# Optimization experiments

Hardware: AMD Instinct MI355X
Metric: run time of the kernel (lower is better)

The kernel has to match this reference:

```python
import jax, jax.numpy as jnp
import numpy as np

K = 16  # top-k patches kept (module default)

def setup_inputs() -> dict:
    key = jax.random.key(0)
    ks = jax.random.split(key, 5)
    N, D, A, H = 100000, 1024, 128, 256
    x = jax.random.normal(ks[0], (N, D), dtype=jnp.float32)
    Wa1 = jax.random.normal(ks[1], (D, A), dtype=jnp.float32) * (1.0 / np.sqrt(D))
    ba1 = jnp.zeros((A,), dtype=jnp.float32)
    Wa2 = jax.random.normal(ks[2], (A, 1), dtype=jnp.float32) * (1.0 / np.sqrt(A))
    ba2 = jnp.zeros((1,), dtype=jnp.float32)
    Wc1 = jax.random.normal(ks[3], (D, H), dtype=jnp.float32) * (1.0 / np.sqrt(D))
    bc1 = jnp.zeros((H,), dtype=jnp.float32)
    Wc2 = jax.random.normal(ks[4], (H, 1), dtype=jnp.float32) * (1.0 / np.sqrt(H))
    bc2 = jnp.zeros((1,), dtype=jnp.float32)
    return {"x": x, "Wa1": Wa1, "ba1": ba1, "Wa2": Wa2, "ba2": ba2,
            "Wc1": Wc1, "bc1": bc1, "Wc2": Wc2, "bc2": bc2}

def reference(x, Wa1, ba1, Wa2, ba2, Wc1, bc1, Wc2, bc2):
    # attention logits: Linear -> tanh -> Linear, shape [N]
    scores = (jnp.tanh(x @ Wa1 + ba1) @ Wa2 + ba2)[:, 0]
    # top-k selection over patch dim (k < N here)
    top_vals, top_idx = jax.lax.top_k(scores, K)       # [K], [K]
    x_k = x[top_idx]                                    # [K, D] gather
    attn_w = jax.nn.softmax(top_vals)                   # renormalise over k
    slide_embedding = attn_w @ x_k                      # [D] weighted sum
    # classifier MLP (dropout is identity in eval)
    h = jax.nn.relu(slide_embedding @ Wc1 + bc1)
    logit = (h @ Wc2 + bc2)[0]
    # scatter attention weights back into full-length vector
    full_weights = jnp.zeros(x.shape[0], dtype=x.dtype).at[top_idx].set(attn_w)
    return logit, slide_embedding, full_weights, top_idx
```

## Files before the change

### kernel.cpp

```cpp
#include <hip/hip_runtime.h>
#include <cstddef>
#include <cstdint>

#define N_PATCH 100000
#define D_IN    1024
#define A_DIM   128
#define H_DIM   256
#define KTOP    16

#define OUT_LOGIT 0
#define OUT_EMB   1
#define OUT_FW    (1 + D_IN)
#define OUT_TOPI  (OUT_FW + N_PATCH)

#define WS_SCORES 0
#define WS_CANDV  (N_PATCH)
#define WS_CANDI  (N_PATCH + 4096)
#define WS_ATTN   (N_PATCH + 2 * 4096)
#define WS_TOPI   (WS_ATTN + KTOP)
#define WS_EMB    (WS_TOPI + KTOP)
#define WS_HPART  (WS_EMB + D_IN)
#define WS_WPK    (WS_HPART + 16 * H_DIM)

#define NB2A  256
#define CHUNK 391

typedef __attribute__((ext_vector_type(8))) short bf8_t;
typedef __attribute__((ext_vector_type(4))) float f4_t;

__global__ __launch_bounds__(256) void k_prepack(
    const float* __restrict__ Wa1, uint4* __restrict__ wpk)
{
    int t = blockIdx.x * 256 + threadIdx.x;
    int lane = t & 63;
    int part = (t >> 6) & 1;
    int nt   = (t >> 7) & 7;
    int ks   = t >> 10;
    int n  = nt * 16 + (lane & 15);
    int k0 = ks * 32 + ((lane >> 4) * 8);
    union { ushort u[8]; uint4 v; } o;
    #pragma unroll
    for (int j = 0; j < 8; ++j) {
        float w = Wa1[(size_t)(k0 + j) * A_DIM + n];
        uint b = __float_as_uint(w);
        if (part == 0) {
            o.u[j] = (ushort)(b >> 16);
        } else {
            float hf = __uint_as_float(b & 0xffff0000u);
            o.u[j] = (ushort)(__float_as_uint(w - hf) >> 16);
        }
    }
    wpk[t] = o.v;
}

__device__ __forceinline__ void split8(const float4& a, const float4& b,
                                       bf8_t& hi, bf8_t& lo)
{
    union { float f[8]; uint u[8]; float4 v4[2]; } X;
    X.v4[0] = a; X.v4[1] = b;
    union { uint u[4]; bf8_t v; } H, L;
    #pragma unroll
    for (int j = 0; j < 4; ++j) {
        uint x0 = X.u[2 * j], x1 = X.u[2 * j + 1];
        H.u[j] = __builtin_amdgcn_perm(x1, x0, 0x07060302);
        float l0 = X.f[2 * j]     - __uint_as_float(x0 & 0xffff0000u);
        float l1 = X.f[2 * j + 1] - __uint_as_float(x1 & 0xffff0000u);
        L.u[j] = __builtin_amdgcn_perm(__float_as_uint(l1), __float_as_uint(l0), 0x07060302);
    }
    hi = H.v; lo = L.v;
}

#define MFMA_BF16 __builtin_amdgcn_mfma_f32_16x16x32_bf16

__global__ __launch_bounds__(256) void k_scores(
    const float* __restrict__ x, const uint4* __restrict__ wpk,
    const float* __restrict__ ba1, const float* __restrict__ Wa2,
    const float* __restrict__ ba2, float* __restrict__ scores)
{
    __shared__ uint4 sB[2][1024];

    const int tid = threadIdx.x;
    const int ln  = tid & 63;
    const int q   = ln >> 4;
    const int c   = ln & 15;
    const int wv  = tid >> 6;
    const int row0 = blockIdx.x * 128 + wv * 32;

    const int r0 = min(row0 + c,      N_PATCH - 1);
    const int r1 = min(row0 + 16 + c, N_PATCH - 1);
    const float* pa0 = x + (size_t)r0 * D_IN + q * 8;
    const float* pa1 = x + (size_t)r1 * D_IN + q * 8;

    f4_t acc[2][8];
    #pragma unroll
    for (int rt = 0; rt < 2; ++rt)
        #pragma unroll
        for (int nt = 0; nt < 8; ++nt)
            acc[rt][nt] = (f4_t){0.f, 0.f, 0.f, 0.f};

    uint4 b0[4], bpre[4];
    #pragma unroll
    for (int i = 0; i < 4; ++i) b0[i] = wpk[tid + i * 256];
    #pragma unroll
    for (int i = 0; i < 4; ++i) sB[0][tid + i * 256] = b0[i];
    #pragma unroll
    for (int i = 0; i < 4; ++i) bpre[i] = wpk[1024 + tid + i * 256];

    float4 a_cur[4], a_nxt[4];
    a_cur[0] = *(const float4*)(pa0);
    a_cur[1] = *(const float4*)(pa0 + 4);
    a_cur[2] = *(const float4*)(pa1);
    a_cur[3] = *(const float4*)(pa1 + 4);

    __syncthreads();

    for (int ks = 0; ks < 32; ++ks) {
        const int cur = ks & 1;

        if (ks < 31) {
            #pragma unroll
            for (int i = 0; i < 4; ++i) sB[cur ^ 1][tid + i * 256] = bpre[i];
            a_nxt[0] = *(const float4*)(pa0 + (ks + 1) * 32);
            a_nxt[1] = *(const float4*)(pa0 + (ks + 1) * 32 + 4);
            a_nxt[2] = *(const float4*)(pa1 + (ks + 1) * 32);
            a_nxt[3] = *(const float4*)(pa1 + (ks + 1) * 32 + 4);
        }
        if (ks < 30) {
            #pragma unroll
            for (int i = 0; i < 4; ++i) bpre[i] = wpk[(ks + 2) * 1024 + tid + i * 256];
        }

        bf8_t ahi0, alo0, ahi1, alo1;
        split8(a_cur[0], a_cur[1], ahi0, alo0);
        split8(a_cur[2], a_cur[3], ahi1, alo1);

        const bf8_t* sBf = (const bf8_t*)sB[cur];
        #pragma unroll
        for (int nt = 0; nt < 8; nt += 2) {
            bf8_t bh0 = sBf[(nt * 2 + 0) * 64 + ln];
            bf8_t bl0 = sBf[(nt * 2 + 1) * 64 + ln];
            bf8_t bh1 = sBf[(nt * 2 + 2) * 64 + ln];
            bf8_t bl1 = sBf[(nt * 2 + 3) * 64 + ln];
            acc[0][nt]     = MFMA_BF16(ahi0, bh0, acc[0][nt],     0, 0, 0);
            acc[1][nt]     = MFMA_BF16(ahi1, bh0, acc[1][nt],     0, 0, 0);
            acc[0][nt + 1] = MFMA_BF16(ahi0, bh1, acc[0][nt + 1], 0, 0, 0);
            acc[1][nt + 1] = MFMA_BF16(ahi1, bh1, acc[1][nt + 1], 0, 0, 0);
            acc[0][nt]     = MFMA_BF16(alo0, bh0, acc[0][nt],     0, 0, 0);
            acc[1][nt]     = MFMA_BF16(alo1, bh0, acc[1][nt],     0, 0, 0);
            acc[0][nt + 1] = MFMA_BF16(alo0, bh1, acc[0][nt + 1], 0, 0, 0);
            acc[1][nt + 1] = MFMA_BF16(alo1, bh1, acc[1][nt + 1], 0, 0, 0);
            acc[0][nt]     = MFMA_BF16(ahi0, bl0, acc[0][nt],     0, 0, 0);
            acc[1][nt]     = MFMA_BF16(ahi1, bl0, acc[1][nt],     0, 0, 0);
            acc[0][nt + 1] = MFMA_BF16(ahi0, bl1, acc[0][nt + 1], 0, 0, 0);
            acc[1][nt + 1] = MFMA_BF16(ahi1, bl1, acc[1][nt + 1], 0, 0, 0);
        }

        #pragma unroll
        for (int i = 0; i < 4; ++i) a_cur[i] = a_nxt[i];
        __syncthreads();
    }

    float b1v[8], w2v[8];
    #pragma unroll
    for (int nt = 0; nt < 8; ++nt) {
        b1v[nt] = ba1[nt * 16 + c];
        w2v[nt] = Wa2[nt * 16 + c];
    }
    const float b2 = ba2[0];

    #pragma unroll
    for (int rt = 0; rt < 2; ++rt)
        #pragma unroll
        for (int reg = 0; reg < 4; ++reg) {
            float p = 0.f;
            #pragma unroll
            for (int nt = 0; nt < 8; ++nt)
                p += tanhf(acc[rt][nt][reg] + b1v[nt]) * w2v[nt];
            #pragma unroll
            for (int off = 1; off < 16; off <<= 1)
                p += __shfl_xor(p, off, 64);
            if (c == 0) {
                int row = row0 + rt * 16 + q * 4 + reg;
                if (row < N_PATCH) scores[row] = p + b2;
            }
        }
}

__global__ __launch_bounds__(256) void k_topk_local(
    const float* __restrict__ scores, float* __restrict__ candv,
    int* __restrict__ candi, float* __restrict__ out_fw)
{
    __shared__ float sv[512];
    __shared__ float rv[256];
    __shared__ int   rs[256];
    const int tid  = threadIdx.x;
    const int base = blockIdx.x * CHUNK;

    for (int i = tid; i < 512; i += 256) {
        int g = base + i;
        sv[i] = (i < CHUNK && g < N_PATCH) ? scores[g] : -1e30f;
    }
    for (int i = tid; i < CHUNK; i += 256) {
        int g = base + i;
        if (g < N_PATCH) out_fw[g] = 0.f;
    }
    __syncthreads();

    for (int r = 0; r < KTOP; ++r) {
        float v1 = sv[tid], v2 = sv[tid + 256];
        float bv; int bs;
        if (v2 > v1) { bv = v2; bs = tid + 256; } else { bv = v1; bs = tid; }
        rv[tid] = bv; rs[tid] = bs;
        __syncthreads();
        for (int off = 128; off > 0; off >>= 1) {
            if (tid < off) {
                float ov = rv[tid + off]; int os = rs[tid + off];
                if (ov > rv[tid] || (ov == rv[tid] && os < rs[tid])) {
                    rv[tid] = ov; rs[tid] = os;
                }
            }
            __syncthreads();
        }
        if (tid == 0) {
            int s = rs[0];
            candv[blockIdx.x * KTOP + r] = rv[0];
            candi[blockIdx.x * KTOP + r] = base + s;
            sv[s] = -1e30f;
        }
        __syncthreads();
    }
}

__global__ __launch_bounds__(256) void k_topk_global(
    const float* __restrict__ candv, const int* __restrict__ candi,
    float* __restrict__ out, float* __restrict__ ws_attn, int* __restrict__ ws_topi)
{
    __shared__ float cv[4096];
    __shared__ int   ci[4096];
    __shared__ float rv[256];
    __shared__ int   rgx[256];
    __shared__ int   rsl[256];
    __shared__ float topv[KTOP];
    __shared__ int   topi[KTOP];
    __shared__ float attn[KTOP];
    const int tid = threadIdx.x;

    for (int i = tid; i < 4096; i += 256) { cv[i] = candv[i]; ci[i] = candi[i]; }
    __syncthreads();

    for (int r = 0; r < KTOP; ++r) {
        float bv = -1e38f; int bg = 0x7fffffff; int bs = tid * 16;
        #pragma unroll
        for (int i = 0; i < 16; ++i) {
            int s = tid * 16 + i;
            float v = cv[s]; int g = ci[s];
            if (v > bv || (v == bv && g < bg)) { bv = v; bg = g; bs = s; }
        }
        rv[tid] = bv; rgx[tid] = bg; rsl[tid] = bs;
        __syncthreads();
        for (int off = 128; off > 0; off >>= 1) {
            if (tid < off) {
                if (rv[tid + off] > rv[tid] ||
                    (rv[tid + off] == rv[tid] && rgx[tid + off] < rgx[tid])) {
                    rv[tid] = rv[tid + off]; rgx[tid] = rgx[tid + off]; rsl[tid] = rsl[tid + off];
                }
            }
            __syncthreads();
        }
        if (tid == 0) {
            topv[r] = rv[0]; topi[r] = rgx[0]; cv[rsl[0]] = -1e30f;
        }
        __syncthreads();
    }

    if (tid == 0) {
        float mx = topv[0];
        float s = 0.f;
        for (int k2 = 0; k2 < KTOP; ++k2) {
            float e = expf(topv[k2] - mx);
            attn[k2] = e; s += e;
        }
        float inv = 1.f / s;
        for (int k2 = 0; k2 < KTOP; ++k2) attn[k2] *= inv;
    }
    __syncthreads();

    if (tid < KTOP) {
        out[OUT_TOPI + tid] = (float)topi[tid];
        out[OUT_FW + topi[tid]] = attn[tid];
        ws_attn[tid] = attn[tid];
        ws_topi[tid] = topi[tid];
    }
}

__global__ __launch_bounds__(256) void k_embed(
    const float* __restrict__ x, const float* __restrict__ attn,
    const int* __restrict__ topi, float* __restrict__ out, float* __restrict__ emb)
{
    __shared__ float a[KTOP];
    __shared__ int   ti[KTOP];
    if (threadIdx.x < KTOP) { a[threadIdx.x] = attn[threadIdx.x]; ti[threadIdx.x] = topi[threadIdx.x]; }
    __syncthreads();
    int d = blockIdx.x * 256 + threadIdx.x;
    float e = 0.f;
    #pragma unroll
    for (int k2 = 0; k2 < KTOP; ++k2)
        e = fmaf(a[k2], x[(size_t)ti[k2] * D_IN + d], e);
    out[OUT_EMB + d] = e;
    emb[d] = e;
}

__global__ __launch_bounds__(256) void k_mlp1(
    const float* __restrict__ emb, const float* __restrict__ Wc1,
    float* __restrict__ hpart)
{
    __shared__ float se[64];
    const int b = blockIdx.x, tid = threadIdx.x;
    if (tid < 64) se[tid] = emb[b * 64 + tid];
    __syncthreads();
    float p = 0.f;
    #pragma unroll 8
    for (int d = 0; d < 64; ++d)
        p = fmaf(se[d], Wc1[(size_t)(b * 64 + d) * H_DIM + tid], p);
    hpart[b * H_DIM + tid] = p;
}

__global__ __launch_bounds__(256) void k_logit(
    const float* __restrict__ hpart, const float* __restrict__ bc1,
    const float* __restrict__ Wc2, const float* __restrict__ bc2,
    float* __restrict__ out)
{
    __shared__ float red[256];
    const int tid = threadIdx.x;
    float h = bc1[tid];
    #pragma unroll
    for (int i = 0; i < 16; ++i) h += hpart[i * H_DIM + tid];
    h = fmaxf(h, 0.f) * Wc2[tid];
    red[tid] = h;
    __syncthreads();
    for (int off = 128; off > 0; off >>= 1) {
        if (tid < off) red[tid] += red[tid + off];
        __syncthreads();
    }
    if (tid == 0) out[OUT_LOGIT] = red[0] + bc2[0];
}

extern "C" void kernel_launch(void* const* d_in, const int* in_sizes, int n_in,
                              void* d_out, int out_size, void* d_ws, size_t ws_size,
                              hipStream_t stream)
{
    const float* x   = (const float*)d_in[0];
    const float* Wa1 = (const float*)d_in[1];
    const float* ba1 = (const float*)d_in[2];
    const float* Wa2 = (const float*)d_in[3];
    const float* ba2 = (const float*)d_in[4];
    const float* Wc1 = (const float*)d_in[5];
    const float* bc1 = (const float*)d_in[6];
    const float* Wc2 = (const float*)d_in[7];
    const float* bc2 = (const float*)d_in[8];
    float* out = (float*)d_out;
    float* ws  = (float*)d_ws;

    float* scores = ws + WS_SCORES;
    float* candv  = ws + WS_CANDV;
    int*   candi  = (int*)(ws + WS_CANDI);
    float* attn   = ws + WS_ATTN;
    int*   topi   = (int*)(ws + WS_TOPI);
    float* emb    = ws + WS_EMB;
    float* hpart  = ws + WS_HPART;
    uint4* wpk    = (uint4*)(ws + WS_WPK);

    dim3 blk(256);
    k_prepack<<<128, blk, 0, stream>>>(Wa1, wpk);
    k_scores<<<(N_PATCH + 127) / 128, blk, 0, stream>>>(x, wpk, ba1, Wa2, ba2, scores);
    k_topk_local<<<NB2A, blk, 0, stream>>>(scores, candv, candi, out + OUT_FW);
    k_topk_global<<<1, blk, 0, stream>>>(candv, candi, out, attn, topi);
    k_embed<<<4, blk, 0, stream>>>(x, attn, topi, out, emb);
    k_mlp1<<<16, blk, 0, stream>>>(emb, Wc1, hpart);
    k_logit<<<1, blk, 0, stream>>>(hpart, bc1, Wc2, bc2, out);
}
```

Measured before the change: 776.8 us.

## Unroll score GEMM by two with register double-buffered A loads; fuse tail kernels

Measured after the change: 785.3 us. Within noise of the previous version (+1.1%).

```diff
diff --git a/kernel.cpp b/kernel.cpp
--- a/kernel.cpp
+++ b/kernel.cpp
@@ -16,11 +16,7 @@
 #define WS_SCORES 0
 #define WS_CANDV  (N_PATCH)
 #define WS_CANDI  (N_PATCH + 4096)
-#define WS_ATTN   (N_PATCH + 2 * 4096)
-#define WS_TOPI   (WS_ATTN + KTOP)
-#define WS_EMB    (WS_TOPI + KTOP)
-#define WS_HPART  (WS_EMB + D_IN)
-#define WS_WPK    (WS_HPART + 16 * H_DIM)
+#define WS_WPK    (N_PATCH + 2 * 4096 + 64)
 
 #define NB2A  256
 #define CHUNK 391
@@ -72,6 +68,52 @@
 
 #define MFMA_BF16 __builtin_amdgcn_mfma_f32_16x16x32_bf16
 
+#define BAR_LDS() do {                                          \
+    asm volatile("s_waitcnt lgkmcnt(0)" ::: "memory");          \
+    __builtin_amdgcn_s_barrier();                               \
+    asm volatile("" ::: "memory");                              \
+} while (0)
+
+#define SCORE_STEP(KS, CUR) do {                                               \
+    bf8_t ahi0, alo0, ahi1, alo1;                                              \
+    split8(A##CUR[0], A##CUR[1], ahi0, alo0);                                  \
+    split8(A##CUR[2], A##CUR[3], ahi1, alo1);                                  \
+    if ((KS) < 31) {                                                           \
+        _Pragma("unroll")                                                      \
+        for (int i = 0; i < 4; ++i) sB[(CUR) ^ 1][tid + i * 256] = bpre[i];    \
+    }                                                                          \
+    {                                                                          \
+        const int kp = ((KS) + 2 < 32) ? (KS) + 2 : 31;                        \
+        _Pragma("unroll")                                                      \
+        for (int i = 0; i < 4; ++i) bpre[i] = wpk[kp * 1024 + tid + i * 256];  \
+        A##CUR[0] = *(const float4*)(pa0 + kp * 32);                           \
+        A##CUR[1] = *(const float4*)(pa0 + kp * 32 + 4);                       \
+        A##CUR[2] = *(const float4*)(pa1 + kp * 32);                           \
+        A##CUR[3] = *(const float4*)(pa1 + kp * 32 + 4);                       \
+    }                                                                          \
+    const bf8_t* sBf = (const bf8_t*)sB[CUR];                                  \
+    _Pragma("unroll")                                                          \
+    for (int nt = 0; nt < 8; nt += 2) {                                        \
+        bf8_t bh0 = sBf[(nt * 2 + 0) * 64 + ln];                               \
+        bf8_t bl0 = sBf[(nt * 2 + 1) * 64 + ln];                               \
+        bf8_t bh1 = sBf[(nt * 2 + 2) * 64 + ln];                               \
+        bf8_t bl1 = sBf[(nt * 2 + 3) * 64 + ln];                               \
+        acc[0][nt]     = MFMA_BF16(ahi0, bh0, acc[0][nt],     0, 0, 0);        \
+        acc[1][nt]     = MFMA_BF16(ahi1, bh0, acc[1][nt],     0, 0, 0);        \
+        acc[0][nt + 1] = MFMA_BF16(ahi0, bh1, acc[0][nt + 1], 0, 0, 0);        \
+        acc[1][nt + 1] = MFMA_BF16(ahi1, bh1, acc[1][nt + 1], 0, 0, 0);        \
+        acc[0][nt]     = MFMA_BF16(alo0, bh0, acc[0][nt],     0, 0, 0);        \
+        acc[1][nt]     = MFMA_BF16(alo1, bh0, acc[1][nt],     0, 0, 0);        \
+        acc[0][nt + 1] = MFMA_BF16(alo0, bh1, acc[0][nt + 1], 0, 0, 0);        \
+        acc[1][nt + 1] = MFMA_BF16(alo1, bh1, acc[1][nt + 1], 0, 0, 0);        \
+        acc[0][nt]     = MFMA_BF16(ahi0, bl0, acc[0][nt],     0, 0, 0);        \
+        acc[1][nt]     = MFMA_BF16(ahi1, bl0, acc[1][nt],     0, 0, 0);        \
+        acc[0][nt + 1] = MFMA_BF16(ahi0, bl1, acc[0][nt + 1], 0, 0, 0);        \
+        acc[1][nt + 1] = MFMA_BF16(ahi1, bl1, acc[1][nt + 1], 0, 0, 0);        \
+    }                                                                          \
+    BAR_LDS();                                                                 \
+} while (0)
+
 __global__ __launch_bounds__(256) void k_scores(
     const float* __restrict__ x, const uint4* __restrict__ wpk,
     const float* __restrict__ ba1, const float* __restrict__ Wa2,
@@ -98,66 +140,32 @@
         for (int nt = 0; nt < 8; ++nt)
             acc[rt][nt] = (f4_t){0.f, 0.f, 0.f, 0.f};
 
-    uint4 b0[4], bpre[4];
-    #pragma unroll
-    for (int i = 0; i < 4; ++i) b0[i] = wpk[tid + i * 256];
-    #pragma unroll
-    for (int i = 0; i < 4; ++i) sB[0][tid + i * 256] = b0[i];
+    uint4 bpre[4];
+    {
+        uint4 b0[4];
+        #pragma unroll
+        for (int i = 0; i < 4; ++i) b0[i] = wpk[tid + i * 256];
+        #pragma unroll
+        for (int i = 0; i < 4; ++i) sB[0][tid + i * 256] = b0[i];
+    }
     #pragma unroll
     for (int i = 0; i < 4; ++i) bpre[i] = wpk[1024 + tid + i * 256];
 
-    float4 a_cur[4], a_nxt[4];
-    a_cur[0] = *(const float4*)(pa0);
-    a_cur[1] = *(const float4*)(pa0 + 4);
-    a_cur[2] = *(const float4*)(pa1);
-    a_cur[3] = *(const float4*)(pa1 + 4);
-
-    __syncthreads();
-
-    for (int ks = 0; ks < 32; ++ks) {
-        const int cur = ks & 1;
-
-        if (ks < 31) {
-            #pragma unroll
-            for (int i = 0; i < 4; ++i) sB[cur ^ 1][tid + i * 256] = bpre[i];
-            a_nxt[0] = *(const float4*)(pa0 + (ks + 1) * 32);
-            a_nxt[1] = *(const float4*)(pa0 + (ks + 1) * 32 + 4);
-            a_nxt[2] = *(const float4*)(pa1 + (ks + 1) * 32);
-            a_nxt[3] = *(const float4*)(pa1 + (ks + 1) * 32 + 4);
-        }
-        if (ks < 30) {
-            #pragma unroll
-            for (int i = 0; i < 4; ++i) bpre[i] = wpk[(ks + 2) * 1024 + tid + i * 256];
-        }
-
-        bf8_t ahi0, alo0, ahi1, alo1;
-        split8(a_cur[0], a_cur[1], ahi0, alo0);
-        split8(a_cur[2], a_cur[3], ahi1, alo1);
-
-        const bf8_t* sBf = (const bf8_t*)sB[cur];
-        #pragma unroll
-        for (int nt = 0; nt < 8; nt += 2) {
-            bf8_t bh0 = sBf[(nt * 2 + 0) * 64 + ln];
-            bf8_t bl0 = sBf[(nt * 2 + 1) * 64 + ln];
-            bf8_t bh1 = sBf[(nt * 2 + 2) * 64 + ln];
-            bf8_t bl1 = sBf[(nt * 2 + 3) * 64 + ln];
-            acc[0][nt]     = MFMA_BF16(ahi0, bh0, acc[0][nt],     0, 0, 0);
-            acc[1][nt]     = MFMA_BF16(ahi1, bh0, acc[1][nt],     0, 0, 0);
-            acc[0][nt + 1] = MFMA_BF16(ahi0, bh1, acc[0][nt + 1], 0, 0, 0);
-            acc[1][nt + 1] = MFMA_BF16(ahi1, bh1, acc[1][nt + 1], 0, 0, 0);
-            acc[0][nt]     = MFMA_BF16(alo0, bh0, acc[0][nt],     0, 0, 0);
-            acc[1][nt]     = MFMA_BF16(alo1, bh0, acc[1][nt],     0, 0, 0);
-            acc[0][nt + 1] = MFMA_BF16(alo0, bh1, acc[0][nt + 1], 0, 0, 0);
-            acc[1][nt + 1] = MFMA_BF16(alo1, bh1, acc[1][nt + 1], 0, 0, 0);
-            acc[0][nt]     = MFMA_BF16(ahi0, bl0, acc[0][nt],     0, 0, 0);
-            acc[1][nt]     = MFMA_BF16(ahi1, bl0, acc[1][nt],     0, 0, 0);
-            acc[0][nt + 1] = MFMA_BF16(ahi0, bl1, acc[0][nt + 1], 0, 0, 0);
-            acc[1][nt + 1] = MFMA_BF16(ahi1, bl1, acc[1][nt + 1], 0, 0, 0);
-        }
-
-        #pragma unroll
-        for (int i = 0; i < 4; ++i) a_cur[i] = a_nxt[i];
-        __syncthreads();
+    float4 A0[4], A1[4];
+    A0[0] = *(const float4*)(pa0);
+    A0[1] = *(const float4*)(pa0 + 4);
+    A0[2] = *(const float4*)(pa1);
+    A0[3] = *(const float4*)(pa1 + 4);
+    A1[0] = *(const float4*)(pa0 + 32);
+    A1[1] = *(const float4*)(pa0 + 36);
+    A1[2] = *(const float4*)(pa1 + 32);
+    A1[3] = *(const float4*)(pa1 + 36);
+
+    BAR_LDS();
+
+    for (int ks = 0; ks < 32; ks += 2) {
+        SCORE_STEP(ks,     0);
+        SCORE_STEP(ks + 1, 1);
     }
 
     float b1v[8], w2v[8];
@@ -231,9 +239,11 @@
     }
 }
 
-__global__ __launch_bounds__(256) void k_topk_global(
+__global__ __launch_bounds__(256) void k_finalize(
     const float* __restrict__ candv, const int* __restrict__ candi,
-    float* __restrict__ out, float* __restrict__ ws_attn, int* __restrict__ ws_topi)
+    const float* __restrict__ x, const float* __restrict__ Wc1,
+    const float* __restrict__ bc1, const float* __restrict__ Wc2,
+    const float* __restrict__ bc2, float* __restrict__ out)
 {
     __shared__ float cv[4096];
     __shared__ int   ci[4096];
@@ -243,6 +253,8 @@
     __shared__ float topv[KTOP];
     __shared__ int   topi[KTOP];
     __shared__ float attn[KTOP];
+    __shared__ float semb[D_IN] __attribute__((aligned(16)));
+    __shared__ float red[256];
     const int tid = threadIdx.x;
 
     for (int i = tid; i < 4096; i += 256) { cv[i] = candv[i]; ci[i] = candi[i]; }
@@ -288,53 +300,34 @@
     if (tid < KTOP) {
         out[OUT_TOPI + tid] = (float)topi[tid];
         out[OUT_FW + topi[tid]] = attn[tid];
-        ws_attn[tid] = attn[tid];
-        ws_topi[tid] = topi[tid];
-    }
-}
-
-__global__ __launch_bounds__(256) void k_embed(
-    const float* __restrict__ x, const float* __restrict__ attn,
-    const int* __restrict__ topi, float* __restrict__ out, float* __restrict__ emb)
-{
-    __shared__ float a[KTOP];
-    __shared__ int   ti[KTOP];
-    if (threadIdx.x < KTOP) { a[threadIdx.x] = attn[threadIdx.x]; ti[threadIdx.x] = topi[threadIdx.x]; }
-    __syncthreads();
-    int d = blockIdx.x * 256 + threadIdx.x;
-    float e = 0.f;
-    #pragma unroll
-    for (int k2 = 0; k2 < KTOP; ++k2)
-        e = fmaf(a[k2], x[(size_t)ti[k2] * D_IN + d], e);
-    out[OUT_EMB + d] = e;
-    emb[d] = e;
-}
-
-__global__ __launch_bounds__(256) void k_mlp1(
-    const float* __restrict__ emb, const float* __restrict__ Wc1,
-    float* __restrict__ hpart)
-{
-    __shared__ float se[64];
-    const int b = blockIdx.x, tid = threadIdx.x;
-    if (tid < 64) se[tid] = emb[b * 64 + tid];
-    __syncthreads();
-    float p = 0.f;
-    #pragma unroll 8
-    for (int d = 0; d < 64; ++d)
-        p = fmaf(se[d], Wc1[(size_t)(b * 64 + d) * H_DIM + tid], p);
-    hpart[b * H_DIM + tid] = p;
-}
-
-__global__ __launch_bounds__(256) void k_logit(
-    const float* __restrict__ hpart, const float* __restrict__ bc1,
-    const float* __restrict__ Wc2, const float* __restrict__ bc2,
-    float* __restrict__ out)
-{
-    __shared__ float red[256];
-    const int tid = threadIdx.x;
-    float h = bc1[tid];
-    #pragma unroll
-    for (int i = 0; i < 16; ++i) h += hpart[i * H_DIM + tid];
+    }
+
+    float4 e = {0.f, 0.f, 0.f, 0.f};
+    #pragma unroll
+    for (int k2 = 0; k2 < KTOP; ++k2) {
+        const float a = attn[k2];
+        const float4 xv = *(const float4*)(x + (size_t)topi[k2] * D_IN + tid * 4);
+        e.x = fmaf(a, xv.x, e.x);
+        e.y = fmaf(a, xv.y, e.y);
+        e.z = fmaf(a, xv.z, e.z);
+        e.w = fmaf(a, xv.w, e.w);
+    }
+    *(float4*)(&semb[tid * 4]) = e;
+    out[OUT_EMB + tid * 4 + 0] = e.x;
+    out[OUT_EMB + tid * 4 + 1] = e.y;
+    out[OUT_EMB + tid * 4 + 2] = e.z;
+    out[OUT_EMB + tid * 4 + 3] = e.w;
+    __syncthreads();
+
+    float p0 = 0.f, p1 = 0.f, p2 = 0.f, p3 = 0.f;
+    #pragma unroll 2
+    for (int d = 0; d < D_IN; d += 4) {
+        p0 = fmaf(semb[d + 0], Wc1[(size_t)(d + 0) * H_DIM + tid], p0);
+        p1 = fmaf(semb[d + 1], Wc1[(size_t)(d + 1) * H_DIM + tid], p1);
+        p2 = fmaf(semb[d + 2], Wc1[(size_t)(d + 2) * H_DIM + tid], p2);
+        p3 = fmaf(semb[d + 3], Wc1[(size_t)(d + 3) * H_DIM + tid], p3);
+    }
+    float h = bc1[tid] + ((p0 + p1) + (p2 + p3));
     h = fmaxf(h, 0.f) * Wc2[tid];
     red[tid] = h;
     __syncthreads();
@@ -364,18 +357,11 @@
     float* scores = ws + WS_SCORES;
     float* candv  = ws + WS_CANDV;
     int*   candi  = (int*)(ws + WS_CANDI);
-    float* attn   = ws + WS_ATTN;
-    int*   topi   = (int*)(ws + WS_TOPI);
-    float* emb    = ws + WS_EMB;
-    float* hpart  = ws + WS_HPART;
     uint4* wpk    = (uint4*)(ws + WS_WPK);
 
     dim3 blk(256);
     k_prepack<<<128, blk, 0, stream>>>(Wa1, wpk);
     k_scores<<<(N_PATCH + 127) / 128, blk, 0, stream>>>(x, wpk, ba1, Wa2, ba2, scores);
     k_topk_local<<<NB2A, blk, 0, stream>>>(scores, candv, candi, out + OUT_FW);
-    k_topk_global<<<1, blk, 0, stream>>>(candv, candi, out, attn, topi);
-    k_embed<<<4, blk, 0, stream>>>(x, attn, topi, out, emb);
-    k_mlp1<<<16, blk, 0, stream>>>(emb, Wc1, hpart);
-    k_logit<<<1, blk, 0, stream>>>(hpart, bc1, Wc2, bc2, out);
-}
+    k_finalize<<<1, blk, 0, stream>>>(candv, candi, x, Wc1, bc1, Wc2, bc2, out);
+}
```
